# Optimization experiments

Measured on AMD Instinct MI355X. Metric: run time of the kernel, lower is better.

The kernel has to match this reference:

```python
import jax, jax.numpy as jnp
import numpy as np

T, V, D = 8, 100000, 128   # tables, rows per table, embedding dim
B = 4096                   # batch (bags per table)
N = 204800                 # total jagged values per table (avg pooling factor 50)


def setup_inputs() -> dict:
    key = jax.random.key(0)
    k1, k2, k3, k4 = jax.random.split(key, 4)
    tables = jax.random.normal(k1, (T, V, D), dtype=jnp.float32) * 0.01
    values = jax.random.randint(k2, (T, N), 0, V, dtype=jnp.int32)
    # offsets per table: [0, sorted interior points, N]  (include_last_offset=True)
    interior = jnp.sort(jax.random.randint(k3, (T, B - 1), 0, N, dtype=jnp.int32), axis=1)
    zeros = jnp.zeros((T, 1), dtype=jnp.int32)
    ends = jnp.full((T, 1), N, dtype=jnp.int32)
    offsets = jnp.concatenate([zeros, interior, ends], axis=1)  # [T, B+1]
    per_sample_weights = jax.random.uniform(k4, (T, N), dtype=jnp.float32)
    return {"tables": tables, "values": values, "offsets": offsets,
            "per_sample_weights": per_sample_weights}


def reference(tables, values, offsets, per_sample_weights):
    # One EmbeddingBag(mode='sum', include_last_offset=True) per table, vmapped.
    n = values.shape[1]

    def one_table(w, vals, offs, psw):
        emb = w[vals] * psw[:, None]                      # [N, D] weighted gather
        # segment id of position i: j s.t. offs[j] <= i < offs[j+1]
        seg = jnp.searchsorted(offs, jnp.arange(n, dtype=offs.dtype), side='right') - 1
        return jax.ops.segment_sum(emb, seg, num_segments=B)  # [B, D]

    pooled = jax.vmap(one_table)(tables, values, offsets, per_sample_weights)  # [T, B, D]
    # concat per-table pooled embeddings along feature dim -> [B, T*D]
    return jnp.transpose(pooled, (1, 0, 2)).reshape(B, T * D)
```

## Files before the change

### kernel.cpp

```cpp
#include <hip/hip_runtime.h>
#include <hip/hip_bf16.h>


namespace {
constexpr int T = 8;
constexpr int V = 100000;
constexpr int D = 128;
constexpr int B = 4096;
constexpr int N = 204800;
}

__global__ __launch_bounds__(256) void grouped_ebag_kernel(
    const float* __restrict__ tables,
    const int* __restrict__ values,
    const int* __restrict__ offsets,
    const float* __restrict__ psw,
    float* __restrict__ out)
{
    const int wave = threadIdx.x >> 6;
    const int lane = threadIdx.x & 63;
    const int bag  = (blockIdx.x << 2) + wave;
    const int t = bag >> 12;
    const int b = bag & (B - 1);
    const int half = lane >> 5;
    const int c4   = lane & 31;

    const int start = offsets[t * (B + 1) + b];
    const int end   = offsets[t * (B + 1) + b + 1];

    const float* __restrict__ tab  = tables + (size_t)t * (V * D);
    const int*   __restrict__ vals = values + (size_t)t * N;
    const float* __restrict__ wgt  = psw    + (size_t)t * N;

    float4 acc = make_float4(0.f, 0.f, 0.f, 0.f);

    const int len  = end - start;
    const int ngrp = len >> 3;

    int   v[4];
    float wv[4];
    if (ngrp > 0) {
#pragma unroll
        for (int j = 0; j < 4; ++j) {
            v[j]  = vals[start + 2 * j + half];
            wv[j] = wgt [start + 2 * j + half];
        }
    }

    int i = start;
    for (int g = 0; g < ngrp; ++g) {
        int   vn[4] = {0, 0, 0, 0};
        float wn[4] = {0.f, 0.f, 0.f, 0.f};
        const int inext = i + 8;
        if (g + 1 < ngrp) {
#pragma unroll
            for (int j = 0; j < 4; ++j) {
                vn[j] = vals[inext + 2 * j + half];
                wn[j] = wgt [inext + 2 * j + half];
            }
        }
#pragma unroll
        for (int j = 0; j < 4; ++j) {
            const float4 e = *(const float4*)(tab + (size_t)v[j] * D + c4 * 4);
            acc.x = fmaf(e.x, wv[j], acc.x);
            acc.y = fmaf(e.y, wv[j], acc.y);
            acc.z = fmaf(e.z, wv[j], acc.z);
            acc.w = fmaf(e.w, wv[j], acc.w);
        }
#pragma unroll
        for (int j = 0; j < 4; ++j) { v[j] = vn[j]; wv[j] = wn[j]; }
        i = inext;
    }

    for (; i + 2 <= end; i += 2) {
        const int   vv = vals[i + half];
        const float ww = wgt [i + half];
        const float4 e = *(const float4*)(tab + (size_t)vv * D + c4 * 4);
        acc.x = fmaf(e.x, ww, acc.x);
        acc.y = fmaf(e.y, ww, acc.y);
        acc.z = fmaf(e.z, ww, acc.z);
        acc.w = fmaf(e.w, ww, acc.w);
    }
    if (i < end && half == 0) {
        const int   vv = vals[i];
        const float ww = wgt [i];
        const float4 e = *(const float4*)(tab + (size_t)vv * D + c4 * 4);
        acc.x = fmaf(e.x, ww, acc.x);
        acc.y = fmaf(e.y, ww, acc.y);
        acc.z = fmaf(e.z, ww, acc.z);
        acc.w = fmaf(e.w, ww, acc.w);
    }

    acc.x += __shfl_xor(acc.x, 32);
    acc.y += __shfl_xor(acc.y, 32);
    acc.z += __shfl_xor(acc.z, 32);
    acc.w += __shfl_xor(acc.w, 32);

    if (half == 0) {
        *(float4*)(out + (size_t)b * (T * D) + t * D + c4 * 4) = acc;
    }
}

extern "C" void kernel_launch(void* const* d_in, const int* in_sizes, int n_in,
                              void* d_out, int out_size, void* d_ws, size_t ws_size,
                              hipStream_t stream) {
    const float* tables  = (const float*)d_in[0];
    const int*   values  = (const int*)d_in[1];
    const int*   offsets = (const int*)d_in[2];
    const float* psw     = (const float*)d_in[3];
    float*       out     = (float*)d_out;

    dim3 grid((T * B) / 4);
    dim3 block(256);
    grouped_ebag_kernel<<<grid, block, 0, stream>>>(tables, values, offsets, psw, out);
}
```

Before: 573.9 us.

## Cooperatively load bag indices per wave and broadcast via readlane with double-buffered gathers

Each wave now loads up to 64 indices and weights of its bag in one coalesced load and hands each row index to the whole wave with readlane, so the per-lane scalar index loads go away. Every lane handles two columns of a row (float2) instead of half-waves splitting rows with float4, which removes the final cross-half shuffle reduction. Row gathers are issued in groups of eight into two alternating register buffers so the next group's loads overlap the FMAs of the current one. The costs are narrower per-lane loads, serial readlane instructions and higher register pressure from the 16 buffered float2 values.

```diff
diff --git a/kernel.cpp b/kernel.cpp
--- a/kernel.cpp
+++ b/kernel.cpp
@@ -1,5 +1,4 @@
 #include <hip/hip_runtime.h>
-#include <hip/hip_bf16.h>
 
 
 namespace {
@@ -8,6 +7,10 @@
 constexpr int D = 128;
 constexpr int B = 4096;
 constexpr int N = 204800;
+}
+
+__device__ __forceinline__ float readlane_f(float v, int l) {
+    return __int_as_float(__builtin_amdgcn_readlane(__float_as_int(v), l));
 }
 
 __global__ __launch_bounds__(256) void grouped_ebag_kernel(
@@ -22,83 +25,62 @@
     const int bag  = (blockIdx.x << 2) + wave;
     const int t = bag >> 12;
     const int b = bag & (B - 1);
-    const int half = lane >> 5;
-    const int c4   = lane & 31;
 
-    const int start = offsets[t * (B + 1) + b];
-    const int end   = offsets[t * (B + 1) + b + 1];
+    int start = offsets[t * (B + 1) + b];
+    int end   = offsets[t * (B + 1) + b + 1];
+    start = __builtin_amdgcn_readfirstlane(start);
+    end   = __builtin_amdgcn_readfirstlane(end);
+    const int len = end - start;
 
     const float* __restrict__ tab  = tables + (size_t)t * (V * D);
-    const int*   __restrict__ vals = values + (size_t)t * N;
-    const float* __restrict__ wgt  = psw    + (size_t)t * N;
+    const int*   __restrict__ vals = values + (size_t)t * N + start;
+    const float* __restrict__ wgt  = psw    + (size_t)t * N + start;
 
-    float4 acc = make_float4(0.f, 0.f, 0.f, 0.f);
+    float2 acc = make_float2(0.f, 0.f);
 
-    const int len  = end - start;
-    const int ngrp = len >> 3;
+    for (int base = 0; base < len; base += 64) {
+        const int rem = len - base;
+        const int m   = rem < 64 ? rem : 64;
 
-    int   v[4];
-    float wv[4];
-    if (ngrp > 0) {
+        const int pos  = base + lane;
+        const int posc = pos < len ? pos : (len - 1);
+        const int   vidx = vals[posc];
+        const float vw   = (pos < len) ? wgt[posc] : 0.f;
+
+        const int ngrp = (m + 7) >> 3;
+
+        float2 bufA[8], bufB[8];
+
+        auto LOAD = [&](float2 (&buf)[8], int g) {
 #pragma unroll
-        for (int j = 0; j < 4; ++j) {
-            v[j]  = vals[start + 2 * j + half];
-            wv[j] = wgt [start + 2 * j + half];
+            for (int j = 0; j < 8; ++j) {
+                const int r   = (g << 3) + j;
+                const int row = __builtin_amdgcn_readlane(vidx, r);
+                buf[j] = *(const float2*)(tab + (size_t)row * D + lane * 2);
+            }
+        };
+        auto FMA = [&](float2 (&buf)[8], int g) {
+#pragma unroll
+            for (int j = 0; j < 8; ++j) {
+                const int r = (g << 3) + j;
+                const float w = readlane_f(vw, r);
+                acc.x = fmaf(buf[j].x, w, acc.x);
+                acc.y = fmaf(buf[j].y, w, acc.y);
+            }
+        };
+
+        LOAD(bufA, 0);
+        int g = 0;
+        for (; g + 2 <= ngrp; g += 2) {
+            LOAD(bufB, g + 1);
+            FMA(bufA, g);
+            if (g + 2 < ngrp) LOAD(bufA, g + 2);
+            FMA(bufB, g + 1);
         }
+        if (g < ngrp) FMA(bufA, g);
     }
 
-    int i = start;
-    for (int g = 0; g < ngrp; ++g) {
-        int   vn[4] = {0, 0, 0, 0};
-        float wn[4] = {0.f, 0.f, 0.f, 0.f};
-        const int inext = i + 8;
-        if (g + 1 < ngrp) {
-#pragma unroll
-            for (int j = 0; j < 4; ++j) {
-                vn[j] = vals[inext + 2 * j + half];
-                wn[j] = wgt [inext + 2 * j + half];
-            }
-        }
-#pragma unroll
-        for (int j = 0; j < 4; ++j) {
-            const float4 e = *(const float4*)(tab + (size_t)v[j] * D + c4 * 4);
-            acc.x = fmaf(e.x, wv[j], acc.x);
-            acc.y = fmaf(e.y, wv[j], acc.y);
-            acc.z = fmaf(e.z, wv[j], acc.z);
-            acc.w = fmaf(e.w, wv[j], acc.w);
-        }
-#pragma unroll
-        for (int j = 0; j < 4; ++j) { v[j] = vn[j]; wv[j] = wn[j]; }
-        i = inext;
-    }
-
-    for (; i + 2 <= end; i += 2) {
-        const int   vv = vals[i + half];
-        const float ww = wgt [i + half];
-        const float4 e = *(const float4*)(tab + (size_t)vv * D + c4 * 4);
-        acc.x = fmaf(e.x, ww, acc.x);
-        acc.y = fmaf(e.y, ww, acc.y);
-        acc.z = fmaf(e.z, ww, acc.z);
-        acc.w = fmaf(e.w, ww, acc.w);
-    }
-    if (i < end && half == 0) {
-        const int   vv = vals[i];
-        const float ww = wgt [i];
-        const float4 e = *(const float4*)(tab + (size_t)vv * D + c4 * 4);
-        acc.x = fmaf(e.x, ww, acc.x);
-        acc.y = fmaf(e.y, ww, acc.y);
-        acc.z = fmaf(e.z, ww, acc.z);
-        acc.w = fmaf(e.w, ww, acc.w);
-    }
-
-    acc.x += __shfl_xor(acc.x, 32);
-    acc.y += __shfl_xor(acc.y, 32);
-    acc.z += __shfl_xor(acc.z, 32);
-    acc.w += __shfl_xor(acc.w, 32);
-
-    if (half == 0) {
-        *(float4*)(out + (size_t)b * (T * D) + t * D + c4 * 4) = acc;
-    }
+    *(float2*)(out + (size_t)b * (T * D) + t * D + lane * 2) = acc;
 }
 
 extern "C" void kernel_launch(void* const* d_in, const int* in_sizes, int n_in,
```

Result: no change. 565.8 us (-1.4%).
